# Kernel optimization log

Hardware: AMD Instinct MI355X
Metric: run time of the kernel (lower is better)

Reference implementation:

```python
import jax, jax.numpy as jnp
import numpy as np

N_BLOCKS = 1_000_000
N_FILES = 10_000
DIM = 128


def setup_inputs() -> dict:
    key = jax.random.key(0)
    k1, k2, k3, k4, k5 = jax.random.split(key, 5)
    h_blk = jax.random.normal(k1, (N_BLOCKS, DIM), dtype=jnp.float32)
    interior = jnp.sort(jax.random.randint(k2, (N_FILES - 1,), 0, N_BLOCKS))
    blk_ptr = jnp.concatenate([jnp.zeros((1,), jnp.int32), interior.astype(jnp.int32), jnp.full((1,), N_BLOCKS, jnp.int32)])
    # learned params: nn.Linear(dim, dim) weight/bias + context vector
    W = jax.random.normal(k3, (DIM, DIM), dtype=jnp.float32) / np.sqrt(DIM)
    b = jax.random.normal(k4, (DIM,), dtype=jnp.float32) * 0.01
    context = jax.random.normal(k5, (DIM,), dtype=jnp.float32)
    return {"h_blk": h_blk, "W": W, "b": b, "context": context, "blk_ptr": blk_ptr}


def reference(h_blk, W, b, context, blk_ptr):
    N = h_blk.shape[0]
    B = blk_ptr.shape[0] - 1  # static number of segments
    # segment id for each block row: row i in [blk_ptr[k], blk_ptr[k+1]) -> k
    seg = jnp.searchsorted(blk_ptr[1:], jnp.arange(N), side="right")
    # scores = tanh(h @ W^T + b) @ context  -> [N]
    scores = jnp.tanh(h_blk @ W.T + b) @ context
    # per-segment stable softmax
    seg_max = jax.ops.segment_max(scores, seg, num_segments=B)
    e = jnp.exp(scores - seg_max[seg])
    denom = jax.ops.segment_sum(e, seg, num_segments=B)
    alpha = e / denom[seg]
    # weighted sum per segment -> [B, dim]; empty segments give zero rows
    h_file = jax.ops.segment_sum(alpha[:, None] * h_blk, seg, num_segments=B)
    return h_file, alpha
```

## Files before the change

kernel.cpp:

```cpp
#include <hip/hip_runtime.h>
#include <stdint.h>


typedef __attribute__((ext_vector_type(8))) short short8;
typedef __attribute__((ext_vector_type(4))) float f32x4;

#define DIM 128
#define WPAD 136

struct __align__(16) SMemA {
  unsigned short W[128 * WPAD];
  unsigned short h[4][16 * WPAD];
  float bias[DIM];
  float ctx[DIM];
  float e[4][16];
};

__device__ inline unsigned short f2b(float f) {
  union { float f; uint32_t i; } v; v.f = f;
  uint32_t r = v.i + 0x7FFFu + ((v.i >> 16) & 1u);
  return (unsigned short)(r >> 16);
}
__device__ inline float tanh_fast(float x) {
  float e2 = __expf(2.0f * x);
  return 1.0f - 2.0f * __builtin_amdgcn_rcpf(e2 + 1.0f);
}
__device__ inline void atomic_add_f32(float* p, float v) {
  __hip_atomic_fetch_add(p, v, __ATOMIC_RELAXED, __HIP_MEMORY_SCOPE_AGENT);
}

__global__ void zero_kernel(float* __restrict__ hf, float* __restrict__ Dg,
                            int n_hf, int n_d) {
  int i = (blockIdx.x * 256 + threadIdx.x) * 4;
  if (i < n_hf) *(float4*)&hf[i] = make_float4(0.f, 0.f, 0.f, 0.f);
  if (i < n_d) {
    if (i + 3 < n_d) *(float4*)&Dg[i] = make_float4(0.f, 0.f, 0.f, 0.f);
    else for (int k = i; k < n_d; ++k) Dg[k] = 0.f;
  }
}

__global__ __launch_bounds__(256, 3) void scores_kernel(
    const float* __restrict__ h_blk,
    const float* __restrict__ Wg,
    const float* __restrict__ bg,
    const float* __restrict__ cg,
    const int* __restrict__ bp,
    float* __restrict__ e_out,
    float* __restrict__ h_file,
    float* __restrict__ Dg,
    int N, int B)
{
  __shared__ SMemA sm;
  const int tid  = threadIdx.x;
  const int wave = tid >> 6;
  const int lane = tid & 63;

  {
    const float4* Wg4 = (const float4*)Wg;
    for (int rep = 0; rep < 16; ++rep) {
      int c = rep * 256 + tid;
      int row  = c >> 5;
      int col4 = (c & 31) * 4;
      float4 v = Wg4[c];
      ushort4 o;
      o.x = f2b(v.x); o.y = f2b(v.y); o.z = f2b(v.z); o.w = f2b(v.w);
      *(ushort4*)&sm.W[row * WPAD + col4] = o;
    }
    if (tid < DIM) { sm.bias[tid] = bg[tid]; sm.ctx[tid] = cg[tid]; }
  }
  __syncthreads();

  const int quad = lane >> 4;
  const int mrow = lane & 15;
  const int hl   = lane >> 5;
  const int dq   = lane & 31;
  const int ntiles = (N + 15) >> 4;
  const int gw = blockIdx.x * 4 + wave;
  const int nw = gridDim.x * 4;
  const int cpw = (ntiles + nw - 1) / nw;
  const int t0 = gw * cpw;
  const int t1 = min(t0 + cpw, ntiles);
  if (t0 >= t1) return;

  const float4* hg4 = (const float4*)h_blk;
  unsigned short* ht = sm.h[wave];
  float* ebuf = sm.e[wave];

  int cur, nxt;
  {
    int r0r = t0 << 4;
    int lo = 0, hi = B;
    while (hi - lo > 1) {
      int mid = (lo + hi) >> 1;
      if (bp[mid] <= r0r) lo = mid; else hi = mid;
    }
    cur = lo; nxt = bp[lo + 1];
  }

  float4 acc = make_float4(0.f, 0.f, 0.f, 0.f);
  float dsum = 0.f;

  auto flushv = [&]() {
    float4 s = acc;
    s.x += __shfl_xor(s.x, 32);
    s.y += __shfl_xor(s.y, 32);
    s.z += __shfl_xor(s.z, 32);
    s.w += __shfl_xor(s.w, 32);
    float dd = dsum + __shfl_xor(dsum, 32);
    if (lane < 32) {
      float* p = &h_file[(size_t)cur * DIM + lane * 4];
      atomic_add_f32(p + 0, s.x);
      atomic_add_f32(p + 1, s.y);
      atomic_add_f32(p + 2, s.z);
      atomic_add_f32(p + 3, s.w);
    }
    if (lane == 0) atomic_add_f32(&Dg[cur], dd);
    acc = make_float4(0.f, 0.f, 0.f, 0.f);
    dsum = 0.f;
  };

  float4 v[8];
  {
    int tb = t0 << 4; int rows = min(16, N - tb);
#pragma unroll
    for (int rep = 0; rep < 8; ++rep) {
      int c = rep * 64 + lane; int row = c >> 5;
      v[rep] = (row < rows) ? hg4[(size_t)(tb + row) * 32 + (c & 31)]
                            : make_float4(0.f, 0.f, 0.f, 0.f);
    }
  }

  for (int t = t0; t < t1; ++t) {
    const int tb = t << 4;
    const int rows = min(16, N - tb);

#pragma unroll
    for (int rep = 0; rep < 8; ++rep) {
      int c = rep * 64 + lane;
      int row  = c >> 5;
      int col4 = (c & 31) * 4;
      ushort4 o;
      o.x = f2b(v[rep].x); o.y = f2b(v[rep].y);
      o.z = f2b(v[rep].z); o.w = f2b(v[rep].w);
      *(ushort4*)&ht[row * WPAD + col4] = o;
    }

    if (t + 1 < t1) {
      int tb2 = (t + 1) << 4; int rows2 = min(16, N - tb2);
#pragma unroll
      for (int rep = 0; rep < 8; ++rep) {
        int c = rep * 64 + lane; int row = c >> 5;
        v[rep] = (row < rows2) ? hg4[(size_t)(tb2 + row) * 32 + (c & 31)]
                               : make_float4(0.f, 0.f, 0.f, 0.f);
      }
    }

    const unsigned short* ar = &ht[mrow * WPAD + quad * 8];
    short8 a0 = *(const short8*)&ar[0];
    short8 a1 = *(const short8*)&ar[32];
    short8 a2 = *(const short8*)&ar[64];
    short8 a3 = *(const short8*)&ar[96];

    float part0 = 0.f, part1 = 0.f, part2 = 0.f, part3 = 0.f;
    for (int nt = 0; nt < 8; ++nt) {
      const unsigned short* wr = &sm.W[(nt * 16 + mrow) * WPAD + quad * 8];
      short8 b0 = *(const short8*)&wr[0];
      short8 b1 = *(const short8*)&wr[32];
      short8 b2 = *(const short8*)&wr[64];
      short8 b3 = *(const short8*)&wr[96];
      f32x4 c = {0.f, 0.f, 0.f, 0.f};
      c = __builtin_amdgcn_mfma_f32_16x16x32_bf16(a0, b0, c, 0, 0, 0);
      c = __builtin_amdgcn_mfma_f32_16x16x32_bf16(a1, b1, c, 0, 0, 0);
      c = __builtin_amdgcn_mfma_f32_16x16x32_bf16(a2, b2, c, 0, 0, 0);
      c = __builtin_amdgcn_mfma_f32_16x16x32_bf16(a3, b3, c, 0, 0, 0);
      float bj = sm.bias[nt * 16 + mrow];
      float cj = sm.ctx[nt * 16 + mrow];
      part0 += tanh_fast(c.x + bj) * cj;
      part1 += tanh_fast(c.y + bj) * cj;
      part2 += tanh_fast(c.z + bj) * cj;
      part3 += tanh_fast(c.w + bj) * cj;
    }
    for (int m = 1; m <= 8; m <<= 1) {
      part0 += __shfl_xor(part0, m);
      part1 += __shfl_xor(part1, m);
      part2 += __shfl_xor(part2, m);
      part3 += __shfl_xor(part3, m);
    }
    float e0 = __expf(fminf(part0, 87.f)), e1 = __expf(fminf(part1, 87.f));
    float e2 = __expf(fminf(part2, 87.f)), e3 = __expf(fminf(part3, 87.f));
    if (mrow == 0) {
      int rb = quad * 4;
      if (rows == 16) {
        *(float4*)&e_out[tb + rb] = make_float4(e0, e1, e2, e3);
      } else {
        if (rb + 0 < rows) e_out[tb + rb + 0] = e0;
        if (rb + 1 < rows) e_out[tb + rb + 1] = e1;
        if (rb + 2 < rows) e_out[tb + rb + 2] = e2;
        if (rb + 3 < rows) e_out[tb + rb + 3] = e3;
      }
      *(float4*)&ebuf[rb] = make_float4(e0, e1, e2, e3);
    }

    if (rows == 16 && nxt - tb >= 16) {
#pragma unroll
      for (int rep = 0; rep < 8; ++rep) {
        int row = rep * 2 + hl;
        float ei = ebuf[row];
        uint2 u = *(const uint2*)&ht[row * WPAD + dq * 4];
        acc.x += ei * __uint_as_float(u.x << 16);
        acc.y += ei * __uint_as_float(u.x & 0xFFFF0000u);
        acc.z += ei * __uint_as_float(u.y << 16);
        acc.w += ei * __uint_as_float(u.y & 0xFFFF0000u);
        dsum += ei;
      }
    } else {
      for (int i = 0; i < rows; ++i) {
        int r = tb + i;
        if (r >= nxt) {
          flushv();
          do { ++cur; nxt = bp[cur + 1]; } while (nxt <= r);
        }
        if ((i & 1) == hl) {
          float ei = ebuf[i];
          uint2 u = *(const uint2*)&ht[i * WPAD + dq * 4];
          acc.x += ei * __uint_as_float(u.x << 16);
          acc.y += ei * __uint_as_float(u.x & 0xFFFF0000u);
          acc.z += ei * __uint_as_float(u.y << 16);
          acc.w += ei * __uint_as_float(u.y & 0xFFFF0000u);
          dsum += ei;
        }
      }
    }
  }
  flushv();
}

__global__ __launch_bounds__(128) void finalize_kernel(
    const int* __restrict__ bp,
    const float* __restrict__ Dg,
    float* __restrict__ h_file,
    float* __restrict__ e_alpha)
{
  const int seg = blockIdx.x;
  const int tid = threadIdx.x;
  const float D = Dg[seg];
  const float rD = (D > 0.f) ? (1.0f / D) : 0.f;
  h_file[(size_t)seg * DIM + tid] *= rD;
  const int r0 = bp[seg];
  const int r1 = bp[seg + 1];
  for (int i = r0 + tid; i < r1; i += 128) {
    e_alpha[i] *= rD;
  }
}

extern "C" void kernel_launch(void* const* d_in, const int* in_sizes, int n_in,
                              void* d_out, int out_size, void* d_ws, size_t ws_size,
                              hipStream_t stream) {
  const float* h_blk = (const float*)d_in[0];
  const float* Wg    = (const float*)d_in[1];
  const float* bg    = (const float*)d_in[2];
  const float* cg    = (const float*)d_in[3];
  const int*   bp    = (const int*)d_in[4];
  const int N = in_sizes[0] / DIM;
  const int B = in_sizes[4] - 1;

  float* out    = (float*)d_out;
  float* h_file = out;
  float* alpha  = out + (size_t)B * DIM;
  float* Dg     = (float*)d_ws;

  const int n_hf = B * DIM;
  const int zero_blocks = (n_hf / 4 + 255) / 256;
  zero_kernel<<<dim3(zero_blocks), dim3(256), 0, stream>>>(h_file, Dg, n_hf, B);
  scores_kernel<<<dim3(768), dim3(256), 0, stream>>>(h_blk, Wg, bg, cg, bp,
                                                     alpha, h_file, Dg, N, B);
  finalize_kernel<<<dim3(B), dim3(128), 0, stream>>>(bp, Dg, h_file, alpha);
}
```

Baseline: 699.4 us.

## Double-buffer h tile prefetch in registers and accumulate from fp32 registers

After: 723.4 us. 3.4% more time.

```diff
diff --git a/kernel.cpp b/kernel.cpp
--- a/kernel.cpp
+++ b/kernel.cpp
@@ -119,119 +119,131 @@
     dsum = 0.f;
   };
 
-  float4 v[8];
+  float4 va[8], vb[8];
   {
-    int tb = t0 << 4; int rows = min(16, N - tb);
+    int tb = t0 << 4; int rows_ = min(16, N - tb);
 #pragma unroll
     for (int rep = 0; rep < 8; ++rep) {
       int c = rep * 64 + lane; int row = c >> 5;
-      v[rep] = (row < rows) ? hg4[(size_t)(tb + row) * 32 + (c & 31)]
-                            : make_float4(0.f, 0.f, 0.f, 0.f);
-    }
-  }
-
-  for (int t = t0; t < t1; ++t) {
-    const int tb = t << 4;
-    const int rows = min(16, N - tb);
-
+      va[rep] = (row < rows_) ? hg4[(size_t)(tb + row) * 32 + (c & 31)]
+                              : make_float4(0.f, 0.f, 0.f, 0.f);
+    }
+  }
+  if (t0 + 1 < t1) {
+    int tb = (t0 + 1) << 4; int rows_ = min(16, N - tb);
 #pragma unroll
     for (int rep = 0; rep < 8; ++rep) {
-      int c = rep * 64 + lane;
-      int row  = c >> 5;
-      int col4 = (c & 31) * 4;
-      ushort4 o;
-      o.x = f2b(v[rep].x); o.y = f2b(v[rep].y);
-      o.z = f2b(v[rep].z); o.w = f2b(v[rep].w);
-      *(ushort4*)&ht[row * WPAD + col4] = o;
-    }
-
-    if (t + 1 < t1) {
-      int tb2 = (t + 1) << 4; int rows2 = min(16, N - tb2);
-#pragma unroll
-      for (int rep = 0; rep < 8; ++rep) {
-        int c = rep * 64 + lane; int row = c >> 5;
-        v[rep] = (row < rows2) ? hg4[(size_t)(tb2 + row) * 32 + (c & 31)]
-                               : make_float4(0.f, 0.f, 0.f, 0.f);
-      }
-    }
-
-    const unsigned short* ar = &ht[mrow * WPAD + quad * 8];
-    short8 a0 = *(const short8*)&ar[0];
-    short8 a1 = *(const short8*)&ar[32];
-    short8 a2 = *(const short8*)&ar[64];
-    short8 a3 = *(const short8*)&ar[96];
-
-    float part0 = 0.f, part1 = 0.f, part2 = 0.f, part3 = 0.f;
-    for (int nt = 0; nt < 8; ++nt) {
-      const unsigned short* wr = &sm.W[(nt * 16 + mrow) * WPAD + quad * 8];
-      short8 b0 = *(const short8*)&wr[0];
-      short8 b1 = *(const short8*)&wr[32];
-      short8 b2 = *(const short8*)&wr[64];
-      short8 b3 = *(const short8*)&wr[96];
-      f32x4 c = {0.f, 0.f, 0.f, 0.f};
-      c = __builtin_amdgcn_mfma_f32_16x16x32_bf16(a0, b0, c, 0, 0, 0);
-      c = __builtin_amdgcn_mfma_f32_16x16x32_bf16(a1, b1, c, 0, 0, 0);
-      c = __builtin_amdgcn_mfma_f32_16x16x32_bf16(a2, b2, c, 0, 0, 0);
-      c = __builtin_amdgcn_mfma_f32_16x16x32_bf16(a3, b3, c, 0, 0, 0);
-      float bj = sm.bias[nt * 16 + mrow];
-      float cj = sm.ctx[nt * 16 + mrow];
-      part0 += tanh_fast(c.x + bj) * cj;
-      part1 += tanh_fast(c.y + bj) * cj;
-      part2 += tanh_fast(c.z + bj) * cj;
-      part3 += tanh_fast(c.w + bj) * cj;
-    }
-    for (int m = 1; m <= 8; m <<= 1) {
-      part0 += __shfl_xor(part0, m);
-      part1 += __shfl_xor(part1, m);
-      part2 += __shfl_xor(part2, m);
-      part3 += __shfl_xor(part3, m);
-    }
-    float e0 = __expf(fminf(part0, 87.f)), e1 = __expf(fminf(part1, 87.f));
-    float e2 = __expf(fminf(part2, 87.f)), e3 = __expf(fminf(part3, 87.f));
-    if (mrow == 0) {
-      int rb = quad * 4;
-      if (rows == 16) {
-        *(float4*)&e_out[tb + rb] = make_float4(e0, e1, e2, e3);
-      } else {
-        if (rb + 0 < rows) e_out[tb + rb + 0] = e0;
-        if (rb + 1 < rows) e_out[tb + rb + 1] = e1;
-        if (rb + 2 < rows) e_out[tb + rb + 2] = e2;
-        if (rb + 3 < rows) e_out[tb + rb + 3] = e3;
-      }
-      *(float4*)&ebuf[rb] = make_float4(e0, e1, e2, e3);
-    }
-
-    if (rows == 16 && nxt - tb >= 16) {
-#pragma unroll
-      for (int rep = 0; rep < 8; ++rep) {
-        int row = rep * 2 + hl;
-        float ei = ebuf[row];
-        uint2 u = *(const uint2*)&ht[row * WPAD + dq * 4];
-        acc.x += ei * __uint_as_float(u.x << 16);
-        acc.y += ei * __uint_as_float(u.x & 0xFFFF0000u);
-        acc.z += ei * __uint_as_float(u.y << 16);
-        acc.w += ei * __uint_as_float(u.y & 0xFFFF0000u);
-        dsum += ei;
-      }
-    } else {
-      for (int i = 0; i < rows; ++i) {
-        int r = tb + i;
-        if (r >= nxt) {
-          flushv();
-          do { ++cur; nxt = bp[cur + 1]; } while (nxt <= r);
-        }
-        if ((i & 1) == hl) {
-          float ei = ebuf[i];
-          uint2 u = *(const uint2*)&ht[i * WPAD + dq * 4];
-          acc.x += ei * __uint_as_float(u.x << 16);
-          acc.y += ei * __uint_as_float(u.x & 0xFFFF0000u);
-          acc.z += ei * __uint_as_float(u.y << 16);
-          acc.w += ei * __uint_as_float(u.y & 0xFFFF0000u);
-          dsum += ei;
-        }
-      }
-    }
-  }
+      int c = rep * 64 + lane; int row = c >> 5;
+      vb[rep] = (row < rows_) ? hg4[(size_t)(tb + row) * 32 + (c & 31)]
+                              : make_float4(0.f, 0.f, 0.f, 0.f);
+    }
+  }
+
+#define TILE_BODY(VC)                                                       \
+  do {                                                                      \
+    const int tb = t << 4;                                                  \
+    const int rows = min(16, N - tb);                                       \
+    _Pragma("unroll")                                                       \
+    for (int rep = 0; rep < 8; ++rep) {                                     \
+      int c = rep * 64 + lane;                                              \
+      int row  = c >> 5;                                                    \
+      int col4 = (c & 31) * 4;                                              \
+      ushort4 o;                                                            \
+      o.x = f2b(VC[rep].x); o.y = f2b(VC[rep].y);                           \
+      o.z = f2b(VC[rep].z); o.w = f2b(VC[rep].w);                           \
+      *(ushort4*)&ht[row * WPAD + col4] = o;                                \
+    }                                                                       \
+    const unsigned short* ar = &ht[mrow * WPAD + quad * 8];                 \
+    short8 a0 = *(const short8*)&ar[0];                                     \
+    short8 a1 = *(const short8*)&ar[32];                                    \
+    short8 a2 = *(const short8*)&ar[64];                                    \
+    short8 a3 = *(const short8*)&ar[96];                                    \
+    float part0 = 0.f, part1 = 0.f, part2 = 0.f, part3 = 0.f;               \
+    for (int nt = 0; nt < 8; ++nt) {                                        \
+      const unsigned short* wr = &sm.W[(nt * 16 + mrow) * WPAD + quad * 8]; \
+      short8 b0 = *(const short8*)&wr[0];                                   \
+      short8 b1 = *(const short8*)&wr[32];                                  \
+      short8 b2 = *(const short8*)&wr[64];                                  \
+      short8 b3 = *(const short8*)&wr[96];                                  \
+      f32x4 cc = {0.f, 0.f, 0.f, 0.f};                                      \
+      cc = __builtin_amdgcn_mfma_f32_16x16x32_bf16(a0, b0, cc, 0, 0, 0);    \
+      cc = __builtin_amdgcn_mfma_f32_16x16x32_bf16(a1, b1, cc, 0, 0, 0);    \
+      cc = __builtin_amdgcn_mfma_f32_16x16x32_bf16(a2, b2, cc, 0, 0, 0);    \
+      cc = __builtin_amdgcn_mfma_f32_16x16x32_bf16(a3, b3, cc, 0, 0, 0);    \
+      float bj = sm.bias[nt * 16 + mrow];                                   \
+      float cj = sm.ctx[nt * 16 + mrow];                                    \
+      part0 += tanh_fast(cc.x + bj) * cj;                                   \
+      part1 += tanh_fast(cc.y + bj) * cj;                                   \
+      part2 += tanh_fast(cc.z + bj) * cj;                                   \
+      part3 += tanh_fast(cc.w + bj) * cj;                                   \
+    }                                                                       \
+    for (int m = 1; m <= 8; m <<= 1) {                                      \
+      part0 += __shfl_xor(part0, m);                                        \
+      part1 += __shfl_xor(part1, m);                                        \
+      part2 += __shfl_xor(part2, m);                                        \
+      part3 += __shfl_xor(part3, m);                                        \
+    }                                                                       \
+    float e0 = __expf(fminf(part0, 87.f)), e1 = __expf(fminf(part1, 87.f)); \
+    float e2 = __expf(fminf(part2, 87.f)), e3 = __expf(fminf(part3, 87.f)); \
+    if (mrow == 0) {                                                        \
+      int rb = quad * 4;                                                    \
+      if (rows == 16) {                                                     \
+        *(float4*)&e_out[tb + rb] = make_float4(e0, e1, e2, e3);            \
+      } else {                                                              \
+        if (rb + 0 < rows) e_out[tb + rb + 0] = e0;                         \
+        if (rb + 1 < rows) e_out[tb + rb + 1] = e1;                         \
+        if (rb + 2 < rows) e_out[tb + rb + 2] = e2;                         \
+        if (rb + 3 < rows) e_out[tb + rb + 3] = e3;                         \
+      }                                                                     \
+      *(float4*)&ebuf[rb] = make_float4(e0, e1, e2, e3);                    \
+    }                                                                       \
+    if (rows == 16 && nxt - tb >= 16) {                                     \
+                            \
+      _Pragma("unroll")                                                     \
+      for (int rep = 0; rep < 8; ++rep) {                                   \
+        float ei = ebuf[rep * 2 + hl];                                      \
+        acc.x += ei * VC[rep].x; acc.y += ei * VC[rep].y;                   \
+        acc.z += ei * VC[rep].z; acc.w += ei * VC[rep].w;                   \
+        dsum += ei;                                                         \
+      }                                                                     \
+    } else {                                                                \
+              \
+      for (int i = 0; i < rows; ++i) {                                      \
+        int r = tb + i;                                                     \
+        if (r >= nxt) {                                                     \
+          flushv();                                                         \
+          do { ++cur; nxt = bp[cur + 1]; } while (nxt <= r);                \
+        }                                                                   \
+        if ((i & 1) == hl) {                                                \
+          float ei = ebuf[i];                                               \
+          uint2 u = *(const uint2*)&ht[i * WPAD + dq * 4];                  \
+          acc.x += ei * __uint_as_float(u.x << 16);                         \
+          acc.y += ei * __uint_as_float(u.x & 0xFFFF0000u);                 \
+          acc.z += ei * __uint_as_float(u.y << 16);                         \
+          acc.w += ei * __uint_as_float(u.y & 0xFFFF0000u);                 \
+          dsum += ei;                                                       \
+        }                                                                   \
+      }                                                                     \
+    }                                                                       \
+    \
+    if (t + 2 < t1) {                                                       \
+      int tb2 = (t + 2) << 4; int rows2 = min(16, N - tb2);                 \
+      _Pragma("unroll")                                                     \
+      for (int rep = 0; rep < 8; ++rep) {                                   \
+        int c = rep * 64 + lane; int row = c >> 5;                          \
+        VC[rep] = (row < rows2) ? hg4[(size_t)(tb2 + row) * 32 + (c & 31)]  \
+                                : make_float4(0.f, 0.f, 0.f, 0.f);          \
+      }                                                                     \
+    }                                                                       \
+  } while (0)
+
+  int t = t0;
+  while (t < t1) {
+    TILE_BODY(va); ++t;
+    if (t >= t1) break;
+    TILE_BODY(vb); ++t;
+  }
+#undef TILE_BODY
   flushv();
 }
 
```
